# Kernel tuning notes

Measured on AMD Instinct MI355X. Metric: run time of the kernel, lower is better.

The kernel has to match this reference:

```python
import jax, jax.numpy as jnp
import numpy as np

B, T, C, NH = 4, 2048, 1024, 16
D = C // NH  # 64


def setup_inputs() -> dict:
    key = jax.random.key(0)
    ks = jax.random.split(key, 6)
    x = jax.random.normal(ks[0], (B, T, C), dtype=jnp.float32)
    # realistic RoPE tables: interleaved cos/sin over T positions, D head dim
    inv_freq = 1.0 / (10000.0 ** (np.arange(0, D, 2, dtype=np.float32) / D))
    ang = np.arange(T, dtype=np.float32)[:, None] * inv_freq[None, :]  # (T, D/2)
    ang = np.repeat(ang, 2, axis=-1)  # (T, D) interleaved
    pe_cos = jnp.asarray(np.cos(ang))[None, None]  # (1,1,T,D)
    pe_sin = jnp.asarray(np.sin(ang))[None, None]
    pe_scale = jax.random.uniform(ks[1], (1, 1, T, D), dtype=jnp.float32, minval=0.5, maxval=1.5)
    mask = 0.1 * jax.random.normal(ks[2], (1, B, T, T), dtype=jnp.float32)
    w_qkv = jax.random.normal(ks[3], (3 * C, C), dtype=jnp.float32) * (C ** -0.5)
    b_qkv = jax.random.normal(ks[4], (3 * C,), dtype=jnp.float32) * 0.02
    return {"x": x, "pe_cos": pe_cos, "pe_sin": pe_sin, "pe_scale": pe_scale,
            "mask": mask, "w_qkv": w_qkv, "b_qkv": b_qkv}


def _rotate_interleaved(u):
    # even positions <- -odd, odd positions <- even (RoPE interleave)
    u2 = u.reshape(u.shape[:-1] + (-1, 2))
    rot = jnp.stack([-u2[..., 1], u2[..., 0]], axis=-1)
    return rot.reshape(u.shape)


def reference(x, pe_cos, pe_sin, pe_scale, mask, w_qkv, b_qkv):
    b, t, c = x.shape
    qkv = x @ w_qkv.T + b_qkv  # (b, t, 3c)
    q, k, v = jnp.split(qkv, 3, axis=-1)
    # (b, t, nh, d) -> (b, nh, t, d)
    to_heads = lambda u: u.reshape(b, t, NH, D).transpose(0, 2, 1, 3)
    q, k, v = to_heads(q), to_heads(k), to_heads(v)
    # pe tensors (1,1,t,d) broadcast over (b,nh,t,d)
    q = (q * pe_cos + _rotate_interleaved(q) * pe_sin) * pe_scale
    k = (k * pe_cos + _rotate_interleaved(k) * pe_sin) / pe_scale
    scale = 1.0 / ((2.0 * D) ** 0.5)  # original uses scale=1/sqrt(2d)
    scores = jnp.einsum('bhqd,bhkd->bhqk', q, k) * scale
    # torch layout was (nh, b, t, t) + mask (1, b, t, t): mask broadcasts over heads
    scores = scores + jnp.swapaxes(mask, 0, 1)  # mask -> (b, 1, t, t)
    attn = jax.nn.softmax(scores, axis=-1)
    out = jnp.einsum('bhqk,bhkd->bhqd', attn, v)  # (b, nh, t, d)
    return out.transpose(0, 2, 1, 3).reshape(b, t, c)
```

## Files before the change

kernel.cpp:

```cpp
#include <hip/hip_runtime.h>
#include <math.h>

#define NB 4
#define NT 2048
#define NC 1024
#define NHEADS 16
#define HDIM 64

typedef __attribute__((ext_vector_type(8))) _Float16 half8v;
typedef __attribute__((ext_vector_type(4))) float f32x4;

__device__ inline unsigned short f2h(float f) {
    _Float16 h = (_Float16)f;
    return __builtin_bit_cast(unsigned short, h);
}
__device__ inline float h2f(unsigned short u) {
    return (float)__builtin_bit_cast(_Float16, u);
}

#define AS1C(p) ((const __attribute__((address_space(1))) unsigned int*)(unsigned long long)(const void*)(p))
#define AS3P(p) ((__attribute__((address_space(3))) unsigned int*)(unsigned int)(unsigned long long)(void*)(p))
#define GLL16(gp, lp) __builtin_amdgcn_global_load_lds(AS1C(gp), AS3P(lp), 16, 0, 0)

__global__ __launch_bounds__(256) void conv_f16_kernel(
    const float* __restrict__ in, unsigned short* __restrict__ out, int n4)
{
    const int i = blockIdx.x * 256 + threadIdx.x;
    if (i >= n4) return;
    const float4 f = ((const float4*)in)[i];
    ushort4 h;
    h.x = f2h(f.x); h.y = f2h(f.y); h.z = f2h(f.z); h.w = f2h(f.w);
    ((ushort4*)out)[i] = h;
}

__global__ __launch_bounds__(256) void qkv_gemm_kernel(
    const unsigned short* __restrict__ xf, const unsigned short* __restrict__ wf,
    const float* __restrict__ bias, const float* __restrict__ pe_cos,
    const float* __restrict__ pe_sin, const float* __restrict__ pe_scale,
    unsigned short* __restrict__ qb, unsigned short* __restrict__ kb,
    unsigned short* __restrict__ vtb)
{
    __shared__ __align__(16) unsigned short Ah[128 * 32];
    __shared__ __align__(16) unsigned short Bh[128 * 32];

    const int tid = threadIdx.x;
    const int w = tid >> 6, lane = tid & 63;
    const int g = lane >> 4, fr = lane & 15;
    const int wr = w >> 1, wc = w & 1;

    const int bid = blockIdx.x;
    const int s = (bid & 7) * 192 + (bid >> 3);
    const int m0 = (s & 63) * 128, n0 = (s >> 6) * 128;

    const int c0 = tid, c1 = tid + 256;
    const int r0 = c0 >> 2, r1 = c1 >> 2;
    const int cb0 = ((c0 & 3) * 16) ^ (((r0 >> 1) & 3) << 4);
    const int cb1 = ((c1 & 3) * 16) ^ (((r1 >> 1) & 3) << 4);
    const unsigned short* px0 = xf + (size_t)(m0 + r0) * NC + (cb0 >> 1);
    const unsigned short* px1 = xf + (size_t)(m0 + r1) * NC + (cb1 >> 1);
    const unsigned short* pw0 = wf + (size_t)(n0 + r0) * NC + (cb0 >> 1);
    const unsigned short* pw1 = wf + (size_t)(n0 + r1) * NC + (cb1 >> 1);

    f32x4 acc[4][4];
#pragma unroll
    for (int m = 0; m < 4; ++m)
#pragma unroll
        for (int n = 0; n < 4; ++n) acc[m][n] = (f32x4){0.f, 0.f, 0.f, 0.f};

    for (int k0 = 0; k0 < NC; k0 += 32) {
        __syncthreads();
        GLL16(px0 + k0, (char*)Ah + c0 * 16);
        GLL16(px1 + k0, (char*)Ah + c1 * 16);
        GLL16(pw0 + k0, (char*)Bh + c0 * 16);
        GLL16(pw1 + k0, (char*)Bh + c1 * 16);
        __syncthreads();

        half8v a_f[4], b_f[4];
#pragma unroll
        for (int m = 0; m < 4; ++m) {
            const int r = wr * 64 + m * 16 + fr;
            const int off = r * 64 + ((g * 16) ^ (((r >> 1) & 3) << 4));
            a_f[m] = *(const half8v*)((const char*)Ah + off);
        }
#pragma unroll
        for (int n = 0; n < 4; ++n) {
            const int r = wc * 64 + n * 16 + fr;
            const int off = r * 64 + ((g * 16) ^ (((r >> 1) & 3) << 4));
            b_f[n] = *(const half8v*)((const char*)Bh + off);
        }
#pragma unroll
        for (int m = 0; m < 4; ++m)
#pragma unroll
            for (int n = 0; n < 4; ++n)
                acc[m][n] = __builtin_amdgcn_mfma_f32_16x16x32_f16(a_f[m], b_f[n], acc[m][n], 0, 0, 0);
    }

#pragma unroll
    for (int n = 0; n < 4; ++n) {
        const int col = n0 + wc * 64 + n * 16 + fr;
        const int part = col >> 10;
        const int hh = (col & 1023) >> 6;
        const int dd = col & 63;
        const float bv = bias[col];
#pragma unroll
        for (int m = 0; m < 4; ++m) {
            const int row0 = m0 + wr * 64 + m * 16 + 4 * g;
            const int bb = row0 >> 11;
            const int t0 = row0 & 2047;
            if (part < 2) {
                unsigned short* outp = (part == 0) ? qb : kb;
#pragma unroll
                for (int j = 0; j < 4; ++j) {
                    const int t = t0 + j;
                    float val = acc[m][n][j] + bv;
                    const float partner = __shfl_xor(val, 1, 64);
                    const int pidx = t * HDIM + dd;
                    const float cc = pe_cos[pidx], ss = pe_sin[pidx], sc = pe_scale[pidx];
                    const float r = (dd & 1) ? (val * cc + partner * ss)
                                             : (val * cc - partner * ss);
                    val = (part == 0) ? (r * sc) : (r / sc);
                    outp[(((size_t)bb * NHEADS + hh) * NT + t) * HDIM + dd] = f2h(val);
                }
            } else {
                ushort4 sv;
                sv.x = f2h(acc[m][n][0] + bv);
                sv.y = f2h(acc[m][n][1] + bv);
                sv.z = f2h(acc[m][n][2] + bv);
                sv.w = f2h(acc[m][n][3] + bv);
                *(ushort4*)&vtb[(((size_t)bb * NHEADS + hh) * HDIM + dd) * NT + t0] = sv;
            }
        }
    }
}

__global__ __launch_bounds__(256) void attn_mfma_kernel(
    const unsigned short* __restrict__ qb, const unsigned short* __restrict__ kb,
    const unsigned short* __restrict__ vtb, const unsigned short* __restrict__ m16,
    float* __restrict__ out)
{
    __shared__ __align__(16) unsigned short Ks[64 * 64];
    __shared__ __align__(16) unsigned short Vs[64 * 64];
    __shared__ __align__(16) unsigned short Ps[4][32 * 64];

    const int tid = threadIdx.x;
    const int w = tid >> 6, lane = tid & 63;
    const int g = lane >> 4, fr = lane & 15;

    const int bid = blockIdx.x;
    const int s = (bid & 7) * 128 + (bid >> 3);
    const int q0 = (s & 15) * 128;
    const int h = (s >> 4) & 15;
    const int b = s >> 8;

    const size_t bh = (size_t)b * NHEADS + h;
    const unsigned short* qp = qb + (bh * NT + q0 + w * 32) * HDIM;
    const unsigned short* kp = kb + bh * NT * HDIM;
    const unsigned short* vtp = vtb + bh * HDIM * NT;
    const unsigned short* mp = m16 + ((size_t)b * NT + q0 + w * 32) * NT;

    half8v qf[2][2];
#pragma unroll
    for (int m = 0; m < 2; ++m)
#pragma unroll
        for (int kk = 0; kk < 2; ++kk)
            qf[m][kk] = *(const half8v*)(qp + (m * 16 + fr) * HDIM + kk * 32 + g * 8);

    f32x4 acc[2][4];
    float li[2][4], mi[2][4];
#pragma unroll
    for (int m = 0; m < 2; ++m)
#pragma unroll
        for (int j = 0; j < 4; ++j) {
            li[m][j] = 0.f; mi[m][j] = -3.0e38f;
            acc[m][j] = (f32x4){0.f, 0.f, 0.f, 0.f};
        }
    const float scl = 0.08838834764831845f;

    for (int kt = 0; kt < NT / 64; ++kt) {
        __syncthreads();
        {
            const unsigned short* ktp = kp + kt * 64 * HDIM;
#pragma unroll
            for (int half = 0; half < 2; ++half) {
                const int c = tid + half * 256;
                const int r = c >> 3;
                const int cb = ((c & 7) * 16) ^ ((r & 7) << 4);
                GLL16(ktp + r * HDIM + (cb >> 1), (char*)Ks + c * 16);
                GLL16(vtp + (size_t)r * NT + kt * 64 + (cb >> 1), (char*)Vs + c * 16);
            }
        }
        __syncthreads();

        half8v kf[4][2];
#pragma unroll
        for (int nt = 0; nt < 4; ++nt) {
            const int r = nt * 16 + fr;
#pragma unroll
            for (int kk = 0; kk < 2; ++kk) {
                const int off = r * 128 + ((kk * 64 + g * 16) ^ ((r & 7) << 4));
                kf[nt][kk] = *(const half8v*)((const char*)Ks + off);
            }
        }

#pragma unroll
        for (int m = 0; m < 2; ++m) {
            f32x4 Sm[4];
#pragma unroll
            for (int nt = 0; nt < 4; ++nt) {
                Sm[nt] = (f32x4){0.f, 0.f, 0.f, 0.f};
#pragma unroll
                for (int kk = 0; kk < 2; ++kk)
                    Sm[nt] = __builtin_amdgcn_mfma_f32_16x16x32_f16(qf[m][kk], kf[nt][kk], Sm[nt], 0, 0, 0);
            }

            float sv[4][4], rmj[4];
#pragma unroll
            for (int j = 0; j < 4; ++j) {
                const unsigned short* mrow =
                    mp + (size_t)(m * 16 + 4 * g + j) * NT + kt * 64 + fr;
#pragma unroll
                for (int nt = 0; nt < 4; ++nt)
                    sv[j][nt] = fmaf(Sm[nt][j], scl, h2f(mrow[nt * 16]));
                rmj[j] = fmaxf(fmaxf(sv[j][0], sv[j][1]), fmaxf(sv[j][2], sv[j][3]));
            }

            const float worst = fmaxf(fmaxf(rmj[0] - mi[m][0], rmj[1] - mi[m][1]),
                                      fmaxf(rmj[2] - mi[m][2], rmj[3] - mi[m][3]));
            if (!__all(worst <= 8.f)) {
#pragma unroll
                for (int j = 0; j < 4; ++j) {
                    float rm = rmj[j];
                    rm = fmaxf(rm, __shfl_xor(rm, 1, 64));
                    rm = fmaxf(rm, __shfl_xor(rm, 2, 64));
                    rm = fmaxf(rm, __shfl_xor(rm, 4, 64));
                    rm = fmaxf(rm, __shfl_xor(rm, 8, 64));
                    const float mnew = fmaxf(mi[m][j], rm);
                    const float alpha = __expf(mi[m][j] - mnew);
                    li[m][j] *= alpha;
#pragma unroll
                    for (int dt = 0; dt < 4; ++dt) acc[m][dt][j] *= alpha;
                    mi[m][j] = mnew;
                }
            }

#pragma unroll
            for (int j = 0; j < 4; ++j) {
                const int prow = m * 16 + 4 * g + j;
                float ps = 0.f;
#pragma unroll
                for (int nt = 0; nt < 4; ++nt) {
                    const float p = __expf(sv[j][nt] - mi[m][j]);
                    const int off = prow * 128 + ((nt * 32 + fr * 2) ^ ((prow & 7) << 4));
                    *(unsigned short*)((char*)Ps[w] + off) = f2h(p);
                    ps += p;
                }
                li[m][j] += ps;
            }
        }

        half8v vf[4][2];
#pragma unroll
        for (int dt = 0; dt < 4; ++dt) {
            const int d = dt * 16 + fr;
#pragma unroll
            for (int kk = 0; kk < 2; ++kk) {
                const int off = d * 128 + ((kk * 64 + g * 16) ^ ((d & 7) << 4));
                vf[dt][kk] = *(const half8v*)((const char*)Vs + off);
            }
        }
#pragma unroll
        for (int m = 0; m < 2; ++m) {
            half8v pf[2];
#pragma unroll
            for (int kk = 0; kk < 2; ++kk) {
                const int off = (m * 16 + fr) * 128 + ((kk * 64 + g * 16) ^ ((fr & 7) << 4));
                pf[kk] = *(const half8v*)((const char*)Ps[w] + off);
            }
#pragma unroll
            for (int dt = 0; dt < 4; ++dt)
#pragma unroll
                for (int kk = 0; kk < 2; ++kk)
                    acc[m][dt] = __builtin_amdgcn_mfma_f32_16x16x32_f16(pf[kk], vf[dt][kk], acc[m][dt], 0, 0, 0);
        }
    }

#pragma unroll
    for (int m = 0; m < 2; ++m)
#pragma unroll
        for (int j = 0; j < 4; ++j) {
            float lt = li[m][j];
            lt += __shfl_xor(lt, 1, 64);
            lt += __shfl_xor(lt, 2, 64);
            lt += __shfl_xor(lt, 4, 64);
            lt += __shfl_xor(lt, 8, 64);
            const float inv = 1.f / lt;
            const int t = q0 + w * 32 + m * 16 + 4 * g + j;
            float* op = out + (((size_t)b * NT + t) * NHEADS + h) * HDIM;
#pragma unroll
            for (int dt = 0; dt < 4; ++dt) op[dt * 16 + fr] = acc[m][dt][j] * inv;
        }
}

extern "C" void kernel_launch(void* const* d_in, const int* in_sizes, int n_in,
                              void* d_out, int out_size, void* d_ws, size_t ws_size,
                              hipStream_t stream) {
    const float* x        = (const float*)d_in[0];
    const float* pe_cos   = (const float*)d_in[1];
    const float* pe_sin   = (const float*)d_in[2];
    const float* pe_scale = (const float*)d_in[3];
    const float* mask     = (const float*)d_in[4];
    const float* w_qkv    = (const float*)d_in[5];
    const float* b_qkv    = (const float*)d_in[6];
    float* out = (float*)d_out;

    unsigned short* ws = (unsigned short*)d_ws;
    const size_t PER = (size_t)NB * NHEADS * NT * HDIM;
    unsigned short* qbuf = ws;
    unsigned short* kbuf = ws + PER;
    unsigned short* vtbuf = ws + 2 * PER;
    unsigned short* xbuf = ws + 3 * PER;
    unsigned short* wbuf = xbuf + (size_t)NB * NT * NC;
    unsigned short* maskbuf = ws + 3 * PER;

    conv_f16_kernel<<<8192, 256, 0, stream>>>(x, xbuf, (NB * NT * NC) / 4);
    conv_f16_kernel<<<3072, 256, 0, stream>>>(w_qkv, wbuf, (3 * NC * NC) / 4);
    qkv_gemm_kernel<<<1536, 256, 0, stream>>>(xbuf, wbuf, b_qkv,
                                              pe_cos, pe_sin, pe_scale,
                                              qbuf, kbuf, vtbuf);
    conv_f16_kernel<<<16384, 256, 0, stream>>>(mask, maskbuf, (NB * NT * NT) / 4);
    attn_mfma_kernel<<<1024, 256, 0, stream>>>(qbuf, kbuf, vtbuf, maskbuf, out);
}
```

Before: 273.4 us.

## Double-buffer K/V tiles in attention and permute fp16 mask for vector loads

The attention kernel now keeps two LDS buffers for K and V. It issues the global-to-LDS loads for the next tile before computing on the current one and uses a single barrier per iteration, so load latency can overlap with the MFMA and softmax work. The mask conversion kernel now writes the fp16 mask in a per-64-column permuted order, so each lane reads its four mask values with one 8-byte load instead of four strided 2-byte loads. In exchange, LDS use grows by 16 KB per block, which may lower occupancy, and the mask converter reads its fp32 input with strided scalar loads.

```diff
diff --git a/kernel.cpp b/kernel.cpp
--- a/kernel.cpp
+++ b/kernel.cpp
@@ -31,6 +31,23 @@
     ushort4 h;
     h.x = f2h(f.x); h.y = f2h(f.y); h.z = f2h(f.z); h.w = f2h(f.w);
     ((ushort4*)out)[i] = h;
+}
+
+__global__ __launch_bounds__(256) void mask_conv_kernel(
+    const float* __restrict__ in, unsigned short* __restrict__ out)
+{
+    const size_t i = (size_t)blockIdx.x * 256 + threadIdx.x;
+    const int row = (int)(i >> 9);
+    const int c4 = (int)(i & 511);
+    const int ktb = c4 >> 4;
+    const int fr = c4 & 15;
+    const float* ip = in + (size_t)row * NT + ktb * 64 + fr;
+    ushort4 o;
+    o.x = f2h(ip[0]);
+    o.y = f2h(ip[16]);
+    o.z = f2h(ip[32]);
+    o.w = f2h(ip[48]);
+    ((ushort4*)out)[i] = o;
 }
 
 __global__ __launch_bounds__(256) void qkv_gemm_kernel(
@@ -138,8 +155,8 @@
     const unsigned short* __restrict__ vtb, const unsigned short* __restrict__ m16,
     float* __restrict__ out)
 {
-    __shared__ __align__(16) unsigned short Ks[64 * 64];
-    __shared__ __align__(16) unsigned short Vs[64 * 64];
+    __shared__ __align__(16) unsigned short Ks[2][64 * 64];
+    __shared__ __align__(16) unsigned short Vs[2][64 * 64];
     __shared__ __align__(16) unsigned short Ps[4][32 * 64];
 
     const int tid = threadIdx.x;
@@ -158,6 +175,21 @@
     const unsigned short* vtp = vtb + bh * HDIM * NT;
     const unsigned short* mp = m16 + ((size_t)b * NT + q0 + w * 32) * NT;
 
+    const int sc0 = tid, sc1 = tid + 256;
+    const int sr0 = sc0 >> 3, scb0 = ((sc0 & 7) * 16) ^ ((sr0 & 7) << 4);
+    const int sr1 = sc1 >> 3, scb1 = ((sc1 & 7) * 16) ^ ((sr1 & 7) << 4);
+
+#define STAGE(buf, kt)                                                          \
+    do {                                                                        \
+        const unsigned short* ktp_ = kp + (kt) * 64 * HDIM;                     \
+        GLL16(ktp_ + sr0 * HDIM + (scb0 >> 1), (char*)Ks[buf] + sc0 * 16);      \
+        GLL16(vtp + (size_t)sr0 * NT + (kt) * 64 + (scb0 >> 1),                 \
+              (char*)Vs[buf] + sc0 * 16);                                       \
+        GLL16(ktp_ + sr1 * HDIM + (scb1 >> 1), (char*)Ks[buf] + sc1 * 16);      \
+        GLL16(vtp + (size_t)sr1 * NT + (kt) * 64 + (scb1 >> 1),                 \
+              (char*)Vs[buf] + sc1 * 16);                                       \
+    } while (0)
+
     half8v qf[2][2];
 #pragma unroll
     for (int m = 0; m < 2; ++m)
@@ -176,20 +208,12 @@
         }
     const float scl = 0.08838834764831845f;
 
+    STAGE(0, 0);
+    __syncthreads();
+    int cur = 0;
+
     for (int kt = 0; kt < NT / 64; ++kt) {
-        __syncthreads();
-        {
-            const unsigned short* ktp = kp + kt * 64 * HDIM;
-#pragma unroll
-            for (int half = 0; half < 2; ++half) {
-                const int c = tid + half * 256;
-                const int r = c >> 3;
-                const int cb = ((c & 7) * 16) ^ ((r & 7) << 4);
-                GLL16(ktp + r * HDIM + (cb >> 1), (char*)Ks + c * 16);
-                GLL16(vtp + (size_t)r * NT + kt * 64 + (cb >> 1), (char*)Vs + c * 16);
-            }
-        }
-        __syncthreads();
+        if (kt + 1 < NT / 64) STAGE(cur ^ 1, kt + 1);
 
         half8v kf[4][2];
 #pragma unroll
@@ -198,7 +222,7 @@
 #pragma unroll
             for (int kk = 0; kk < 2; ++kk) {
                 const int off = r * 128 + ((kk * 64 + g * 16) ^ ((r & 7) << 4));
-                kf[nt][kk] = *(const half8v*)((const char*)Ks + off);
+                kf[nt][kk] = *(const half8v*)((const char*)Ks[cur] + off);
             }
         }
 
@@ -216,11 +240,12 @@
             float sv[4][4], rmj[4];
 #pragma unroll
             for (int j = 0; j < 4; ++j) {
-                const unsigned short* mrow =
-                    mp + (size_t)(m * 16 + 4 * g + j) * NT + kt * 64 + fr;
-#pragma unroll
-                for (int nt = 0; nt < 4; ++nt)
-                    sv[j][nt] = fmaf(Sm[nt][j], scl, h2f(mrow[nt * 16]));
+                const ushort4 mv = *(const ushort4*)(
+                    mp + (size_t)(m * 16 + 4 * g + j) * NT + kt * 64 + fr * 4);
+                sv[j][0] = fmaf(Sm[0][j], scl, h2f(mv.x));
+                sv[j][1] = fmaf(Sm[1][j], scl, h2f(mv.y));
+                sv[j][2] = fmaf(Sm[2][j], scl, h2f(mv.z));
+                sv[j][3] = fmaf(Sm[3][j], scl, h2f(mv.w));
                 rmj[j] = fmaxf(fmaxf(sv[j][0], sv[j][1]), fmaxf(sv[j][2], sv[j][3]));
             }
 
@@ -265,7 +290,7 @@
 #pragma unroll
             for (int kk = 0; kk < 2; ++kk) {
                 const int off = d * 128 + ((kk * 64 + g * 16) ^ ((d & 7) << 4));
-                vf[dt][kk] = *(const half8v*)((const char*)Vs + off);
+                vf[dt][kk] = *(const half8v*)((const char*)Vs[cur] + off);
             }
         }
 #pragma unroll
@@ -282,6 +307,9 @@
                 for (int kk = 0; kk < 2; ++kk)
                     acc[m][dt] = __builtin_amdgcn_mfma_f32_16x16x32_f16(pf[kk], vf[dt][kk], acc[m][dt], 0, 0, 0);
         }
+
+        __syncthreads();
+        cur ^= 1;
     }
 
 #pragma unroll
@@ -327,6 +355,6 @@
     qkv_gemm_kernel<<<1536, 256, 0, stream>>>(xbuf, wbuf, b_qkv,
                                               pe_cos, pe_sin, pe_scale,
                                               qbuf, kbuf, vtbuf);
-    conv_f16_kernel<<<16384, 256, 0, stream>>>(mask, maskbuf, (NB * NT * NT) / 4);
+    mask_conv_kernel<<<16384, 256, 0, stream>>>(mask, maskbuf);
     attn_mfma_kernel<<<1024, 256, 0, stream>>>(qbuf, kbuf, vtbuf, maskbuf, out);
 }
```

New measurement: 260.6 us. 4.7% less time.
